# Performance work log

Hardware: AMD Instinct MI355X
Metric: run time of the kernel (lower is better)

Reference implementation:

```python
import jax, jax.numpy as jnp
import numpy as np

B, S, DIN, PPOS = 2, 128, 768, 256
DCAT = 2 * (DIN + PPOS)   # 2048, BiLSTM input dim
H = DCAT // 2             # 1024, LSTM hidden per direction
MAXLEN = 128              # position embedding table size


def _xavier(k, shape):
    lim = float(np.sqrt(6.0 / (shape[0] + shape[1])))
    return jax.random.uniform(k, shape, jnp.float32, -lim, lim)


def _lstm_u(k, shape):
    lim = float(1.0 / np.sqrt(H))
    return jax.random.uniform(k, shape, jnp.float32, -lim, lim)


def setup_inputs() -> dict:
    key = jax.random.key(0)
    ks = jax.random.split(key, 17)
    inp = {
        "input_embeddings": jax.random.normal(ks[0], (B, S, DIN), jnp.float32),
        "pos_emb": _xavier(ks[1], (MAXLEN, PPOS)),
    }
    i = 2
    for l in (0, 1):
        for d in ("f", "b"):
            inp[f"w_ih_l{l}_{d}"] = _lstm_u(ks[i], (4 * H, DCAT)); i += 1
            inp[f"b_ih_l{l}_{d}"] = _lstm_u(ks[i], (4 * H,)); i += 1
            inp[f"b_hh_l{l}_{d}"] = _lstm_u(ks[i], (4 * H,)); i += 1
    inp["fc_w"] = _lstm_u(ks[i], (1, 2 * H)); i += 1
    inp["fc_b"] = _lstm_u(ks[i], (1,))
    inp["convo_len"] = S
    return inp


def _lstm_dir(x, w_ih, b_ih, b_hh):
    # single timestep, h0=c0=0 -> recurrent term vanishes (grad wrt W_hh is 0)
    g = x @ w_ih.T + b_ih + b_hh            # [N, 4H], pytorch gate order i,f,g,o
    i, f, c, o = jnp.split(g, 4, axis=-1)
    cell = jax.nn.sigmoid(i) * jnp.tanh(c)  # f-gate multiplies c0=0
    return jax.nn.sigmoid(o) * jnp.tanh(cell)


def reference(input_embeddings, pos_emb,
              w_ih_l0_f, b_ih_l0_f, b_hh_l0_f,
              w_ih_l0_b, b_ih_l0_b, b_hh_l0_b,
              w_ih_l1_f, b_ih_l1_f, b_hh_l1_f,
              w_ih_l1_b, b_ih_l1_b, b_hh_l1_b,
              fc_w, fc_b, convo_len):
    # positions indexed by int(norm(embedding)) as in the original code
    idx = jnp.linalg.norm(input_embeddings, axis=-1).astype(jnp.int32)  # [B,S]
    e = jnp.concatenate([input_embeddings, pos_emb[idx]], axis=-1)      # [B,S,D']
    # pair (i,j) -> concat(e_i, e_j)
    left = jnp.repeat(e, S, axis=1)          # [B, S*S, D'], row i repeated S times
    right = jnp.tile(e, (1, S, 1))           # [B, S*S, D'], sequence tiled S times
    p = jnp.concatenate([left, right], axis=-1).reshape(B * S * S, DCAT)
    h1 = jnp.concatenate([
        _lstm_dir(p, w_ih_l0_f, b_ih_l0_f, b_hh_l0_f),
        _lstm_dir(p, w_ih_l0_b, b_ih_l0_b, b_hh_l0_b)], axis=-1)        # [N, 2H]
    h2 = jnp.concatenate([
        _lstm_dir(h1, w_ih_l1_f, b_ih_l1_f, b_hh_l1_f),
        _lstm_dir(h1, w_ih_l1_b, b_ih_l1_b, b_hh_l1_b)], axis=-1)       # [N, 2H]
    logits = h2 @ fc_w.T + fc_b              # [N, 1]
    return logits.reshape(B, S * S)
```

## Files before the change

### kernel.cpp

```cpp
#include <hip/hip_runtime.h>
#include <cstdint>

typedef _Float16 f16;
typedef f16   f16x8 __attribute__((ext_vector_type(8)));
typedef f16   f16x4 __attribute__((ext_vector_type(4)));
typedef float f32x4 __attribute__((ext_vector_type(4)));
typedef float f32x8 __attribute__((ext_vector_type(8)));
typedef int   i32x4 __attribute__((ext_vector_type(4)));
typedef signed char c8x8 __attribute__((ext_vector_type(8)));
typedef unsigned int u32;


static constexpr size_t OFF_E16  = 0;
static constexpr size_t OFF_W0P  = 524288;
static constexpr size_t OFF_UV   = 34078720;
static constexpr size_t OFF_B0   = 50855936;
static constexpr size_t OFF_W1P  = 50888704;
static constexpr size_t OFF_B1   = 76054528;
static constexpr size_t OFF_H1   = 76079104;
static constexpr size_t OFF_PART = 210296832;

__device__ __forceinline__ void gl_lds16(const void* g, void* l) {
  __builtin_amdgcn_global_load_lds((const __attribute__((address_space(1))) u32*)g,
                                   (__attribute__((address_space(3))) u32*)l, 16, 0, 0);
}
__device__ __forceinline__ float sigm(float x) { return 1.f / (1.f + __expf(-x)); }
__device__ __forceinline__ float tanh_f(float x) {
  float e = __expf(-2.f * fabsf(x));
  float t = (1.f - e) / (1.f + e);
  return x < 0.f ? -t : t;
}


__global__ __launch_bounds__(256) void prep_e(const float* __restrict__ x,
                                              const float* __restrict__ pos,
                                              f16* __restrict__ e16) {
  int row = blockIdx.x;
  const float* xr = x + (size_t)row * 768;
  double ss = 0.0;
  for (int i = threadIdx.x; i < 768; i += 256) { float v = xr[i]; ss += (double)v * v; }
  __shared__ double red[256];
  red[threadIdx.x] = ss;
  __syncthreads();
  for (int s2 = 128; s2 > 0; s2 >>= 1) {
    if (threadIdx.x < s2) red[threadIdx.x] += red[threadIdx.x + s2];
    __syncthreads();
  }
  __shared__ int idx_s;
  if (threadIdx.x == 0) {
    int idx = (int)((float)sqrt(red[0]));
    idx_s = idx < 0 ? 0 : (idx > 127 ? 127 : idx);
  }
  __syncthreads();
  int idx = idx_s;
  for (int i = threadIdx.x; i < 1024; i += 256) {
    float v = (i < 768) ? xr[i] : pos[idx * 256 + (i - 768)];
    e16[(size_t)row * 1024 + i] = (f16)v;
  }
}

__global__ __launch_bounds__(256) void prep_w0(const float* __restrict__ w0f,
                                               const float* __restrict__ w0b,
                                               f16* __restrict__ w0p) {
  int t = blockIdx.x * 256 + threadIdx.x;
  int n = t >> 8;
  int k4 = (t & 255) * 4;
  int half = n >> 13;
  int nn = n & 8191;
  int d = nn >> 12;
  int r = nn & 4095;
  const float* w = d ? w0b : w0f;
  float4 v = *(const float4*)(w + (size_t)r * 2048 + half * 1024 + k4);
  f16x4 o;
  o[0] = (f16)v.x; o[1] = (f16)v.y; o[2] = (f16)v.z; o[3] = (f16)v.w;
  *(f16x4*)(w0p + (size_t)n * 1024 + k4) = o;
}

__global__ __launch_bounds__(256) void prep_w1(const float* __restrict__ w1f,
                                               const float* __restrict__ w1b,
                                               signed char* __restrict__ w1q) {
  int t = blockIdx.x * 256 + threadIdx.x;
  int n = t >> 8;
  int c8 = (t & 255) * 8;
  int ct = n / 192, r = n % 192;
  int wn = r / 48, r2 = r % 48;
  int g = r2 >> 4, hs = r2 & 15;
  int d = ct >> 4;
  int h = (ct & 15) * 64 + wn * 16 + hs;
  int gsel = (g == 0) ? 0 : (g + 1);
  const float* w = d ? w1b : w1f;
  const float* src = w + (size_t)(gsel * 1024 + h) * 2048 + c8;
  float4 v0 = *(const float4*)(src);
  float4 v1 = *(const float4*)(src + 4);
  c8x8 o;
  o[0] = (signed char)(int)rintf(v0.x * 4064.f);
  o[1] = (signed char)(int)rintf(v0.y * 4064.f);
  o[2] = (signed char)(int)rintf(v0.z * 4064.f);
  o[3] = (signed char)(int)rintf(v0.w * 4064.f);
  o[4] = (signed char)(int)rintf(v1.x * 4064.f);
  o[5] = (signed char)(int)rintf(v1.y * 4064.f);
  o[6] = (signed char)(int)rintf(v1.z * 4064.f);
  o[7] = (signed char)(int)rintf(v1.w * 4064.f);
  *(c8x8*)(w1q + (size_t)n * 2048 + c8) = o;
}

__global__ void prep_bias(const float* bi0f, const float* bh0f,
                          const float* bi0b, const float* bh0b,
                          const float* bi1f, const float* bh1f,
                          const float* bi1b, const float* bh1b,
                          float* bias0, float* bias1) {
  int i = blockIdx.x * 256 + threadIdx.x;
  if (i < 8192) {
    int d = i >> 12, r = i & 4095;
    bias0[i] = d ? (bi0b[r] + bh0b[r]) : (bi0f[r] + bh0f[r]);
  } else if (i < 8192 + 6144) {
    int n = i - 8192;
    int d = n / 3072, rem = n % 3072;
    int g3 = rem >> 10, k = rem & 1023;
    int gsel = (g3 == 0) ? 0 : (g3 + 1);
    int r = gsel * 1024 + k;
    bias1[n] = d ? (bi1b[r] + bh1b[r]) : (bi1f[r] + bh1f[r]);
  }
}

__global__ __launch_bounds__(256) void gemm_l0(const f16* __restrict__ e16,
                                               const f16* __restrict__ w0p,
                                               float* __restrict__ uv) {
  __shared__ __align__(16) f16 As[8192];
  __shared__ __align__(16) f16 Bs[8192];
  int n0 = blockIdx.x * 128;
  int m0 = blockIdx.y * 128;
  int tid = threadIdx.x, lane = tid & 63, w = tid >> 6;
  int wr = (w >> 1) * 64, wc = (w & 1) * 64;
  f32x4 acc[4][4] = {};

  for (int k0 = 0; k0 < 1024; k0 += 64) {
    __syncthreads();
#pragma unroll
    for (int q = 0; q < 4; q++) {
      int ch = tid + q * 256;
      int c = ch >> 7, r = ch & 127;
      gl_lds16(e16 + (size_t)(m0 + r) * 1024 + k0 + c * 8, (char*)As + ch * 16);
    }
#pragma unroll
    for (int q = 0; q < 4; q++) {
      int ch = tid + q * 256;
      int c = ch >> 7, r = ch & 127;
      gl_lds16(w0p + (size_t)(n0 + r) * 1024 + k0 + c * 8, (char*)Bs + ch * 16);
    }
    __syncthreads();
#pragma unroll
    for (int ks = 0; ks < 2; ks++) {
      int cb = ks * 4 + (lane >> 4);
      f16x8 a[4], b[4];
#pragma unroll
      for (int f = 0; f < 4; f++)
        a[f] = *(const f16x8*)(As + (cb * 128 + wr + f * 16 + (lane & 15)) * 8);
#pragma unroll
      for (int g = 0; g < 4; g++)
        b[g] = *(const f16x8*)(Bs + (cb * 128 + wc + g * 16 + (lane & 15)) * 8);
#pragma unroll
      for (int f = 0; f < 4; f++)
#pragma unroll
        for (int g = 0; g < 4; g++)
          acc[f][g] = __builtin_amdgcn_mfma_f32_16x16x32_f16(a[f], b[g], acc[f][g], 0, 0, 0);
    }
  }
  int col = lane & 15, lg = lane >> 4;
#pragma unroll
  for (int f = 0; f < 4; f++)
#pragma unroll
    for (int g = 0; g < 4; g++)
#pragma unroll
      for (int j = 0; j < 4; j++) {
        int row = m0 + wr + f * 16 + lg * 4 + j;
        int c = n0 + wc + g * 16 + col;
        uv[(size_t)row * 16384 + c] = acc[f][g][j];
      }
}

__global__ __launch_bounds__(256) void pair_h1(const float* __restrict__ uv,
                                               const float* __restrict__ bias0,
                                               signed char* __restrict__ h1q) {
  int bi = blockIdx.x >> 2;
  int jbase = (blockIdx.x & 3) * 32;
  int b = bi >> 7;
  int t = threadIdx.x;
  int u = t * 8;
  int dd = u >> 10, k = u & 1023;
  const float* ub = uv + (size_t)bi * 16384 + dd * 4096 + k;
  const float* bb = bias0 + dd * 4096 + k;
  f32x8 gi0 = *(const f32x8*)(ub);
  f32x8 gc0 = *(const f32x8*)(ub + 2048);
  f32x8 go0 = *(const f32x8*)(ub + 3072);
  f32x8 bi8 = *(const f32x8*)(bb);
  f32x8 bc8 = *(const f32x8*)(bb + 2048);
  f32x8 bo8 = *(const f32x8*)(bb + 3072);
#pragma unroll
  for (int e = 0; e < 8; e++) { gi0[e] += bi8[e]; gc0[e] += bc8[e]; go0[e] += bo8[e]; }
  const float* vbase = uv + (size_t)(b << 7) * 16384 + 8192 + dd * 4096 + k;
  signed char* obase = h1q + ((size_t)bi * 128 + jbase) * 2048 + u;
#pragma unroll 2
  for (int j = 0; j < 32; ++j) {
    const float* vb = vbase + (size_t)(jbase + j) * 16384;
    f32x8 vi = *(const f32x8*)(vb);
    f32x8 vc = *(const f32x8*)(vb + 2048);
    f32x8 vo = *(const f32x8*)(vb + 3072);
    c8x8 ov;
#pragma unroll
    for (int e = 0; e < 8; e++) {
      float gi = gi0[e] + vi[e];
      float gc = gc0[e] + vc[e];
      float go = go0[e] + vo[e];
      float cell = sigm(gi) * tanh_f(gc);
      float hv = sigm(go) * tanh_f(cell);
      ov[e] = (signed char)(int)rintf(hv * 127.f);
    }
    *(c8x8*)(obase + (size_t)j * 2048) = ov;
  }
}

__global__ __launch_bounds__(256, 3) void gemm_l1(const signed char* __restrict__ h1q,
                                                  const signed char* __restrict__ w1q,
                                                  const float* __restrict__ bias1,
                                                  const float* __restrict__ fcw,
                                                  float* __restrict__ partial) {
  __shared__ __align__(16) signed char As[3][8192];
  __shared__ __align__(16) signed char Bs[2][12288];
  int bid = blockIdx.x + (blockIdx.y << 5);
  int xcd = bid & 7, idx = bid >> 3;
  int ct = (xcd << 2) | (idx & 3);
  int m0 = (idx >> 2) << 7;
  int d = ct >> 4;
  int tid = threadIdx.x, lane = tid & 63;
  int wn = tid >> 6;
  int la = lane & 15, lq = lane >> 4;
  int lh = la >> 1, lb = la & 1;
  int sA = (lb * 4 + lq) ^ lh;

  const signed char* asrc[2]; signed char* adst[2];
#pragma unroll
  for (int q = 0; q < 2; q++) {
    int ch = tid + q * 256, L = ch >> 3, s = ch & 7;
    int e = s ^ (L & 7), R = 2 * L + (e >> 2), c = e & 3;
    asrc[q] = h1q + (size_t)(m0 + R) * 2048 + c * 16;
    adst[q] = &As[0][ch * 16];
  }
  const signed char* bsrc[3]; signed char* bdst[3];
#pragma unroll
  for (int q = 0; q < 3; q++) {
    int ch = tid + q * 256, L = ch >> 3, s = ch & 7;
    int e = s ^ (L & 7), P = 2 * L + (e >> 2), c = e & 3;
    bsrc[q] = w1q + (size_t)(ct * 192 + P) * 2048 + c * 16;
    bdst[q] = &Bs[0][ch * 16];
  }
  auto stageA = [&](int t, int buf) {
#pragma unroll
    for (int q = 0; q < 2; q++) gl_lds16(asrc[q] + t * 64, adst[q] + buf * 8192);
  };
  auto stageB = [&](int t, int buf) {
#pragma unroll
    for (int q = 0; q < 3; q++) gl_lds16(bsrc[q] + t * 64, bdst[q] + buf * 12288);
  };

  i32x4 acc[8][3] = {};
  stageA(0, 0); stageB(0, 0); stageA(1, 1);
  asm volatile("s_waitcnt vmcnt(2)" ::: "memory");
  __builtin_amdgcn_s_barrier();

  int ab = 0;
  for (int t = 0; t < 32; ++t) {
    const signed char* Ab = &As[ab][0];
    const signed char* Bb = &Bs[t & 1][0];
    i32x4 af[8], bf[3];
#pragma unroll
    for (int rf = 0; rf < 8; rf++)
      af[rf] = *(const i32x4*)(Ab + ((rf * 8 + lh) * 8 + sA) * 16);
#pragma unroll
    for (int cf = 0; cf < 3; cf++)
      bf[cf] = *(const i32x4*)(Bb + ((wn * 24 + cf * 8 + lh) * 8 + sA) * 16);
    if (t < 31) stageB(t + 1, (t + 1) & 1);
    if (t < 30) stageA(t + 2, ab >= 1 ? ab - 1 : ab + 2);
    __builtin_amdgcn_s_setprio(1);
#pragma unroll
    for (int rf = 0; rf < 8; rf++)
#pragma unroll
      for (int cf = 0; cf < 3; cf++)
        acc[rf][cf] = __builtin_amdgcn_mfma_i32_16x16x64_i8(af[rf], bf[cf], acc[rf][cf], 0, 0, 0);
    __builtin_amdgcn_s_setprio(0);
    if (t < 30)      { asm volatile("s_waitcnt vmcnt(2)" ::: "memory"); }
    else             { asm volatile("s_waitcnt vmcnt(0)" ::: "memory"); }
    __builtin_amdgcn_sched_barrier(0);
    __builtin_amdgcn_s_barrier();
    ab = (ab == 2) ? 0 : ab + 1;
  }

  float* sred = (float*)&As[0][0];
  const float S = 1.0f / 516128.0f;
  int hcol = (ct & 15) * 64 + wn * 16 + la;
  float bi = bias1[(d * 3 + 0) * 1024 + hcol];
  float bc = bias1[(d * 3 + 1) * 1024 + hcol];
  float bo = bias1[(d * 3 + 2) * 1024 + hcol];
  float wf = fcw[d * 1024 + hcol];
#pragma unroll
  for (int rf = 0; rf < 8; rf++) {
#pragma unroll
    for (int j = 0; j < 4; j++) {
      float gi = (float)acc[rf][0][j] * S + bi;
      float gc = (float)acc[rf][1][j] * S + bc;
      float go = (float)acc[rf][2][j] * S + bo;
      float cell = sigm(gi) * tanh_f(gc);
      float hv = sigm(go) * tanh_f(cell);
      float v = hv * wf;
      v += __shfl_xor(v, 1);
      v += __shfl_xor(v, 2);
      v += __shfl_xor(v, 4);
      v += __shfl_xor(v, 8);
      if (la == 0) sred[wn * 128 + rf * 16 + lq * 4 + j] = v;
    }
  }
  __syncthreads();
  if (tid < 128) {
    float s = sred[tid] + sred[128 + tid] + sred[256 + tid] + sred[384 + tid];
    partial[(size_t)ct * 32768 + m0 + tid] = s;
  }
}

__global__ void reduce_out(const float* __restrict__ partial,
                           const float* __restrict__ fcb,
                           float* __restrict__ out) {
  int m = blockIdx.x * 256 + threadIdx.x;
  float s = fcb[0];
#pragma unroll
  for (int ct = 0; ct < 32; ct++) s += partial[(size_t)ct * 32768 + m];
  out[m] = s;
}

extern "C" void kernel_launch(void* const* d_in, const int* in_sizes, int n_in,
                              void* d_out, int out_size, void* d_ws, size_t ws_size,
                              hipStream_t stream) {
  const float* x    = (const float*)d_in[0];
  const float* pos  = (const float*)d_in[1];
  const float* w0f  = (const float*)d_in[2];
  const float* bi0f = (const float*)d_in[3];
  const float* bh0f = (const float*)d_in[4];
  const float* w0b  = (const float*)d_in[5];
  const float* bi0b = (const float*)d_in[6];
  const float* bh0b = (const float*)d_in[7];
  const float* w1f  = (const float*)d_in[8];
  const float* bi1f = (const float*)d_in[9];
  const float* bh1f = (const float*)d_in[10];
  const float* w1b  = (const float*)d_in[11];
  const float* bi1b = (const float*)d_in[12];
  const float* bh1b = (const float*)d_in[13];
  const float* fcw  = (const float*)d_in[14];
  const float* fcb  = (const float*)d_in[15];
  float* out = (float*)d_out;

  char* ws = (char*)d_ws;
  f16*   e16   = (f16*)(ws + OFF_E16);
  f16*   w0p   = (f16*)(ws + OFF_W0P);
  float* uv    = (float*)(ws + OFF_UV);
  float* bias0 = (float*)(ws + OFF_B0);
  signed char* w1q = (signed char*)(ws + OFF_W1P);
  float* bias1 = (float*)(ws + OFF_B1);
  signed char* h1q = (signed char*)(ws + OFF_H1);
  float* part  = (float*)(ws + OFF_PART);

  prep_e<<<256, 256, 0, stream>>>(x, pos, e16);
  prep_w0<<<16384, 256, 0, stream>>>(w0f, w0b, w0p);
  prep_w1<<<6144, 256, 0, stream>>>(w1f, w1b, w1q);
  prep_bias<<<56, 256, 0, stream>>>(bi0f, bh0f, bi0b, bh0b, bi1f, bh1f, bi1b, bh1b,
                                    bias0, bias1);
  gemm_l0<<<dim3(128, 2), 256, 0, stream>>>(e16, w0p, uv);
  pair_h1<<<1024, 256, 0, stream>>>(uv, bias0, h1q);
  gemm_l1<<<dim3(32, 256), 256, 0, stream>>>(h1q, w1q, bias1, fcw, part);
  reduce_out<<<128, 256, 0, stream>>>(part, fcb, out);
}
```

Before: 691.4 us.

## Double-buffer gemm_l1 with unified staging and simplify pair_h1 to one row per block

The int8 layer-1 GEMM drops from three A-tile LDS buffers to two. It issues A and B prefetch for the next k-step together and waits for all loads each iteration. The smaller LDS footprint lets the launch bound allow four blocks per CU instead of three, at the cost of shallower prefetch depth and a full vmcnt drain every step. pair_h1 now launches one block per output pair row, and each block reloads its u and bias vectors instead of looping over 32 j values. This raises block count and trades extra cached reads for simpler code.

```diff
diff --git a/kernel.cpp b/kernel.cpp
--- a/kernel.cpp
+++ b/kernel.cpp
@@ -182,50 +182,44 @@
 __global__ __launch_bounds__(256) void pair_h1(const float* __restrict__ uv,
                                                const float* __restrict__ bias0,
                                                signed char* __restrict__ h1q) {
-  int bi = blockIdx.x >> 2;
-  int jbase = (blockIdx.x & 3) * 32;
-  int b = bi >> 7;
+  int row = blockIdx.x;
+  int urow = row >> 7;
+  int b = row >> 14;
+  int vrow = (b << 7) | (row & 127);
   int t = threadIdx.x;
   int u = t * 8;
-  int dd = u >> 10, k = u & 1023;
-  const float* ub = uv + (size_t)bi * 16384 + dd * 4096 + k;
-  const float* bb = bias0 + dd * 4096 + k;
-  f32x8 gi0 = *(const f32x8*)(ub);
-  f32x8 gc0 = *(const f32x8*)(ub + 2048);
-  f32x8 go0 = *(const f32x8*)(ub + 3072);
-  f32x8 bi8 = *(const f32x8*)(bb);
-  f32x8 bc8 = *(const f32x8*)(bb + 2048);
-  f32x8 bo8 = *(const f32x8*)(bb + 3072);
-#pragma unroll
-  for (int e = 0; e < 8; e++) { gi0[e] += bi8[e]; gc0[e] += bc8[e]; go0[e] += bo8[e]; }
-  const float* vbase = uv + (size_t)(b << 7) * 16384 + 8192 + dd * 4096 + k;
-  signed char* obase = h1q + ((size_t)bi * 128 + jbase) * 2048 + u;
-#pragma unroll 2
-  for (int j = 0; j < 32; ++j) {
-    const float* vb = vbase + (size_t)(jbase + j) * 16384;
-    f32x8 vi = *(const f32x8*)(vb);
-    f32x8 vc = *(const f32x8*)(vb + 2048);
-    f32x8 vo = *(const f32x8*)(vb + 3072);
-    c8x8 ov;
-#pragma unroll
-    for (int e = 0; e < 8; e++) {
-      float gi = gi0[e] + vi[e];
-      float gc = gc0[e] + vc[e];
-      float go = go0[e] + vo[e];
-      float cell = sigm(gi) * tanh_f(gc);
-      float hv = sigm(go) * tanh_f(cell);
-      ov[e] = (signed char)(int)rintf(hv * 127.f);
-    }
-    *(c8x8*)(obase + (size_t)j * 2048) = ov;
-  }
-}
-
-__global__ __launch_bounds__(256, 3) void gemm_l1(const signed char* __restrict__ h1q,
+  int d = u >> 10, k = u & 1023;
+  const float* ub = uv + (size_t)urow * 16384 + d * 4096 + k;
+  const float* vb = uv + (size_t)vrow * 16384 + 8192 + d * 4096 + k;
+  const float* bb = bias0 + d * 4096 + k;
+  f32x8 ui = *(const f32x8*)(ub);
+  f32x8 uc = *(const f32x8*)(ub + 2048);
+  f32x8 uo = *(const f32x8*)(ub + 3072);
+  f32x8 vi = *(const f32x8*)(vb);
+  f32x8 vc = *(const f32x8*)(vb + 2048);
+  f32x8 vo = *(const f32x8*)(vb + 3072);
+  f32x8 bi = *(const f32x8*)(bb);
+  f32x8 bc = *(const f32x8*)(bb + 2048);
+  f32x8 bo = *(const f32x8*)(bb + 3072);
+  c8x8 ov;
+#pragma unroll
+  for (int e = 0; e < 8; e++) {
+    float gi = ui[e] + vi[e] + bi[e];
+    float gc = uc[e] + vc[e] + bc[e];
+    float go = uo[e] + vo[e] + bo[e];
+    float cell = sigm(gi) * tanh_f(gc);
+    float hv = sigm(go) * tanh_f(cell);
+    ov[e] = (signed char)(int)rintf(hv * 127.f);
+  }
+  *(c8x8*)(h1q + (size_t)row * 2048 + u) = ov;
+}
+
+__global__ __launch_bounds__(256, 4) void gemm_l1(const signed char* __restrict__ h1q,
                                                   const signed char* __restrict__ w1q,
                                                   const float* __restrict__ bias1,
                                                   const float* __restrict__ fcw,
                                                   float* __restrict__ partial) {
-  __shared__ __align__(16) signed char As[3][8192];
+  __shared__ __align__(16) signed char As[2][8192];
   __shared__ __align__(16) signed char Bs[2][12288];
   int bid = blockIdx.x + (blockIdx.y << 5);
   int xcd = bid & 7, idx = bid >> 3;
@@ -254,24 +248,23 @@
     bsrc[q] = w1q + (size_t)(ct * 192 + P) * 2048 + c * 16;
     bdst[q] = &Bs[0][ch * 16];
   }
-  auto stageA = [&](int t, int buf) {
+  auto stage = [&](int t, int buf) {
 #pragma unroll
     for (int q = 0; q < 2; q++) gl_lds16(asrc[q] + t * 64, adst[q] + buf * 8192);
-  };
-  auto stageB = [&](int t, int buf) {
 #pragma unroll
     for (int q = 0; q < 3; q++) gl_lds16(bsrc[q] + t * 64, bdst[q] + buf * 12288);
   };
 
   i32x4 acc[8][3] = {};
-  stageA(0, 0); stageB(0, 0); stageA(1, 1);
-  asm volatile("s_waitcnt vmcnt(2)" ::: "memory");
+  stage(0, 0);
+  asm volatile("s_waitcnt vmcnt(0)" ::: "memory");
   __builtin_amdgcn_s_barrier();
 
-  int ab = 0;
   for (int t = 0; t < 32; ++t) {
-    const signed char* Ab = &As[ab][0];
-    const signed char* Bb = &Bs[t & 1][0];
+    int cur = t & 1;
+    if (t < 31) stage(t + 1, cur ^ 1);
+    const signed char* Ab = &As[cur][0];
+    const signed char* Bb = &Bs[cur][0];
     i32x4 af[8], bf[3];
 #pragma unroll
     for (int rf = 0; rf < 8; rf++)
@@ -279,8 +272,6 @@
 #pragma unroll
     for (int cf = 0; cf < 3; cf++)
       bf[cf] = *(const i32x4*)(Bb + ((wn * 24 + cf * 8 + lh) * 8 + sA) * 16);
-    if (t < 31) stageB(t + 1, (t + 1) & 1);
-    if (t < 30) stageA(t + 2, ab >= 1 ? ab - 1 : ab + 2);
     __builtin_amdgcn_s_setprio(1);
 #pragma unroll
     for (int rf = 0; rf < 8; rf++)
@@ -288,11 +279,9 @@
       for (int cf = 0; cf < 3; cf++)
         acc[rf][cf] = __builtin_amdgcn_mfma_i32_16x16x64_i8(af[rf], bf[cf], acc[rf][cf], 0, 0, 0);
     __builtin_amdgcn_s_setprio(0);
-    if (t < 30)      { asm volatile("s_waitcnt vmcnt(2)" ::: "memory"); }
-    else             { asm volatile("s_waitcnt vmcnt(0)" ::: "memory"); }
+    asm volatile("s_waitcnt vmcnt(0)" ::: "memory");
     __builtin_amdgcn_sched_barrier(0);
     __builtin_amdgcn_s_barrier();
-    ab = (ab == 2) ? 0 : ab + 1;
   }
 
   float* sred = (float*)&As[0][0];
@@ -373,7 +362,7 @@
   prep_bias<<<56, 256, 0, stream>>>(bi0f, bh0f, bi0b, bh0b, bi1f, bh1f, bi1b, bh1b,
                                     bias0, bias1);
   gemm_l0<<<dim3(128, 2), 256, 0, stream>>>(e16, w0p, uv);
-  pair_h1<<<1024, 256, 0, stream>>>(uv, bias0, h1q);
+  pair_h1<<<32768, 256, 0, stream>>>(uv, bias0, h1q);
   gemm_l1<<<dim3(32, 256), 256, 0, stream>>>(h1q, w1q, bias1, fcw, part);
   reduce_out<<<128, 256, 0, stream>>>(part, fcb, out);
 }
```

Result: slower. 2.078 ms (+200.5%).
